# Kernel optimization log

Measured on AMD Instinct MI355X. Metric: run time of the kernel, lower is better.

## Reference

```python
import jax, jax.numpy as jnp
import numpy as np

BN_EPS = 1e-5

def _bn_eval(x, gamma, beta):
    # Fresh torch BatchNorm1d in eval mode: running_mean=0, running_var=1
    return x * (gamma / jnp.sqrt(1.0 + BN_EPS)) + beta

def setup_inputs() -> dict:
    key = jax.random.key(0)
    ks = jax.random.split(key, 10)
    Q, K, H, W, D = 64, 128, 24, 8, 128
    L = H * W            # seq_len = 192
    FF = 2048            # dim_feedforward
    q_feat = jax.random.normal(ks[0], (Q, H, W, D), dtype=jnp.float32)
    g_feat = jax.random.normal(ks[1], (K, H, W, D), dtype=jnp.float32)
    se = jax.random.normal(ks[2], (L, L), dtype=jnp.float32)
    score_embed = (se + se.T).reshape(1, 1, L, L)
    s = 1.0 / np.sqrt(D)
    fc0_w = jax.random.uniform(ks[3], (D, D), jnp.float32, -s, s)
    fc0_b = jax.random.uniform(ks[4], (D,), jnp.float32, -s, s)
    s2 = 1.0 / np.sqrt(L)
    fc2_w = jax.random.uniform(ks[5], (FF, L), jnp.float32, -s2, s2)
    fc2_b = jax.random.uniform(ks[6], (FF,), jnp.float32, -s2, s2)
    s3 = 1.0 / np.sqrt(FF)
    fc3_w = jax.random.uniform(ks[7], (1, FF), jnp.float32, -s3, s3)
    fc3_b = jax.random.uniform(ks[8], (1,), jnp.float32, -s3, s3)
    bn1_g = jnp.ones((1,)); bn1_b = jnp.zeros((1,))
    bn2_g = jnp.ones((FF,)) + 0.1 * jax.random.normal(ks[9], (FF,), jnp.float32)
    bn2_b = jnp.zeros((FF,))
    bn3_g = jnp.ones((1,)); bn3_b = jnp.zeros((1,))
    return dict(q_feat=q_feat, g_feat=g_feat, score_embed=score_embed,
                fc0_w=fc0_w, fc0_b=fc0_b, fc2_w=fc2_w, fc2_b=fc2_b,
                fc3_w=fc3_w, fc3_b=fc3_b, bn1_g=bn1_g, bn1_b=bn1_b,
                bn2_g=bn2_g, bn2_b=bn2_b, bn3_g=bn3_g, bn3_b=bn3_b)

def reference(q_feat, g_feat, score_embed, fc0_w, fc0_b, fc2_w, fc2_b,
              fc3_w, fc3_b, bn1_g, bn1_b, bn2_g, bn2_b, bn3_g, bn3_b):
    Q = q_feat.shape[0]
    K = g_feat.shape[0]
    D = q_feat.shape[-1]
    L = score_embed.shape[-1]  # seq_len
    tgt = q_feat.reshape(Q, L, D)
    mem = g_feat.reshape(K, L, D)
    query = tgt @ fc0_w.T + fc0_b      # [Q, L, D]
    key_ = mem @ fc0_w.T + fc0_b       # [K, L, D]
    # [Q, K, L(s), L(t)] score, modulated by broadcast sigmoid bias
    score = jnp.einsum('qtd,ksd->qkst', query, key_) * jax.nn.sigmoid(score_embed)
    score = score.reshape(Q * K, L, L)
    # max over s and over t, concatenated per pair -> [QK, 2L]
    score = jnp.concatenate([score.max(axis=1), score.max(axis=2)], axis=-1)
    score = score.reshape(-1, L)       # [2*QK, L]
    score = _bn_eval(score, bn1_g, bn1_b)
    score = score @ fc2_w.T + fc2_b    # [2*QK, FF]
    score = _bn_eval(score, bn2_g, bn2_b)
    score = jax.nn.relu(score)
    score = score @ fc3_w.T + fc3_b    # [2*QK, 1]
    score = score.reshape(-1, 2).sum(axis=-1, keepdims=True)  # [QK, 1]
    score = _bn_eval(score, bn3_g, bn3_b)
    return score.reshape(Q, K)
```

## Files before the change

### kernel.cpp

```cpp
#include <hip/hip_runtime.h>

#define LL 192
#define FF 2048

typedef __attribute__((__ext_vector_type__(8)))  __bf16 bf16x8;
typedef __attribute__((__ext_vector_type__(4)))  __bf16 bf16x4;
typedef __attribute__((__ext_vector_type__(4)))  float  f32x4;

#define MFMA16(a, b, c) __builtin_amdgcn_mfma_f32_16x16x32_bf16((a), (b), (c), 0, 0, 0)


__device__ __forceinline__ float fmax_quad(float x) {
    int xi = __builtin_bit_cast(int, x);
    float y = fmaxf(x, __builtin_bit_cast(float,
                  __builtin_amdgcn_mov_dpp(xi, 0xB1, 0xF, 0xF, true)));
    int yi = __builtin_bit_cast(int, y);
    return fmaxf(y, __builtin_bit_cast(float,
                  __builtin_amdgcn_mov_dpp(yi, 0x4E, 0xF, 0xF, true)));
}

__launch_bounds__(256, 2)
__global__ void proj_prep_kernel(const float* __restrict__ qf_in,
                                 const float* __restrict__ gf_in,
                                 const float* __restrict__ fc0w,
                                 const float* __restrict__ fc0b,
                                 const float* __restrict__ se,
                                 const float* __restrict__ fc2w,
                                 const float* __restrict__ fc2b,
                                 const float* __restrict__ bn2g,
                                 const float* __restrict__ bn2b,
                                 const float* __restrict__ fc3w,
                                 __bf16* __restrict__ kfragA,
                                 __bf16* __restrict__ qfrag16,
                                 float* __restrict__ sig32,
                                 __bf16* __restrict__ fc2w_bf,
                                 float* __restrict__ h2,
                                 float* __restrict__ bb2,
                                 float* __restrict__ f3)
{
    int bx = blockIdx.x, tid = threadIdx.x;
    if (bx >= 1152) {
        int i0 = (bx - 1152) * 256 + tid;
        const int stride = 160 * 256;
        const float c1 = rsqrtf(1.f + 1e-5f);
        for (int i = i0; i < LL * LL; i += stride) {
            int r = i & 3, lane = (i >> 2) & 63, tile = i >> 8;
            int jt = tile % 12, st = tile / 12;
            int s = st * 16 + (lane >> 4) * 4 + r;
            int t = jt * 16 + (lane & 15);
            sig32[i] = 1.f / (1.f + __expf(-se[s * 192 + t]));
        }
        for (int i = i0; i < FF * LL; i += stride)
            fc2w_bf[i] = (__bf16)fc2w[i];
        for (int i = i0; i < FF; i += stride) {
            float h = bn2g[i] * c1;
            h2[i]  = h;
            bb2[i] = fc2b[i] * h + bn2b[i];
            f3[i]  = fc3w[i];
        }
        return;
    }
    __shared__ __bf16 Xs[32][136];
    __shared__ __bf16 Ws[128][136];
    __shared__ __bf16 Os[4096];
    const float* src = (bx < 384) ? (qf_in + (size_t)bx * (32 * 128))
                                  : (gf_in + (size_t)(bx - 384) * (32 * 128));
#pragma unroll
    for (int it = 0; it < 4; ++it) {
        int e = (it * 256 + tid) * 4;
        int r = e >> 7, c = e & 127;
        float4 v = *reinterpret_cast<const float4*>(src + e);
        bf16x4 xv;
        xv[0] = (__bf16)v.x; xv[1] = (__bf16)v.y;
        xv[2] = (__bf16)v.z; xv[3] = (__bf16)v.w;
        *reinterpret_cast<bf16x4*>(&Xs[r][c]) = xv;
    }
#pragma unroll
    for (int it = 0; it < 16; ++it) {
        int e = (it * 256 + tid) * 4;
        int r = e >> 7, c = e & 127;
        float4 v = *reinterpret_cast<const float4*>(fc0w + e);
        bf16x4 xv;
        xv[0] = (__bf16)v.x; xv[1] = (__bf16)v.y;
        xv[2] = (__bf16)v.z; xv[3] = (__bf16)v.w;
        *reinterpret_cast<bf16x4*>(&Ws[r][c]) = xv;
    }
    __syncthreads();

    int wv = tid >> 6, lane = tid & 63, quad = lane >> 4, l16 = lane & 15;
    int n0 = wv * 32;
    f32x4 acc[2][2];
#pragma unroll
    for (int m = 0; m < 2; ++m)
#pragma unroll
        for (int n = 0; n < 2; ++n) acc[m][n] = (f32x4){0.f, 0.f, 0.f, 0.f};
#pragma unroll
    for (int ks = 0; ks < 4; ++ks) {
        bf16x8 a0 = *reinterpret_cast<const bf16x8*>(&Xs[l16][ks * 32 + quad * 8]);
        bf16x8 a1 = *reinterpret_cast<const bf16x8*>(&Xs[16 + l16][ks * 32 + quad * 8]);
        bf16x8 b0 = *reinterpret_cast<const bf16x8*>(&Ws[n0 + l16][ks * 32 + quad * 8]);
        bf16x8 b1 = *reinterpret_cast<const bf16x8*>(&Ws[n0 + 16 + l16][ks * 32 + quad * 8]);
        acc[0][0] = MFMA16(a0, b0, acc[0][0]);
        acc[0][1] = MFMA16(a0, b1, acc[0][1]);
        acc[1][0] = MFMA16(a1, b0, acc[1][0]);
        acc[1][1] = MFMA16(a1, b1, acc[1][1]);
    }
#pragma unroll
    for (int mt = 0; mt < 2; ++mt)
#pragma unroll
        for (int nt = 0; nt < 2; ++nt) {
            int d = n0 + nt * 16 + l16;
            float bv = fc0b[d];
            int abase = mt * 2048 + (d >> 5) * 512 + ((d >> 3) & 3) * 128 + (d & 7);
#pragma unroll
            for (int r = 0; r < 4; ++r)
                Os[abase + (quad * 4 + r) * 8] = (__bf16)(acc[mt][nt][r] + bv);
        }
    __syncthreads();

    int row0 = bx * 32;
    __bf16* dst;
    if (bx < 384) {
        int qi = row0 / 192, tg0 = (row0 % 192) >> 4;
        dst = qfrag16 + qi * 24576 + tg0 * 2048;
    } else {
        int rk0 = row0 - 12288;
        int ki = rk0 / 192, sg0 = (rk0 % 192) >> 4;
        dst = kfragA + ki * 24576 + sg0 * 2048;
    }
#pragma unroll
    for (int it = 0; it < 2; ++it) {
        int e = (it * 256 + tid) * 8;
        *reinterpret_cast<bf16x8*>(dst + e) =
            *reinterpret_cast<const bf16x8*>(&Os[e]);
    }
}

__launch_bounds__(256, 1)
__global__ void score_kernel(const __bf16* __restrict__ kfragA,
                             const __bf16* __restrict__ qfrag16,
                             const float* __restrict__ sig32,
                             const float* __restrict__ bn1g,
                             const float* __restrict__ bn1b,
                             __bf16* __restrict__ Sred)
{
    __shared__ __bf16 Abuf[8192];
    __shared__ __bf16 rowT4[2][16][200];

    int tid = threadIdx.x;
    int q0 = (blockIdx.x & 31) * 2;
    int kbase = (blockIdx.x >> 5) << 2;
    int w = tid >> 6, lane = tid & 63, quad = lane >> 4, l16 = lane & 15;
    const float g1c = bn1g[0] * rsqrtf(1.f + 1e-5f);
    const float b1v = bn1b[0];

    bf16x8 Bf[2][3][4];
#pragma unroll
    for (int p = 0; p < 2; ++p) {
        const __bf16* qb = qfrag16 + (size_t)(q0 + p) * 24576 + lane * 8;
#pragma unroll
        for (int j = 0; j < 3; ++j)
#pragma unroll
            for (int ks = 0; ks < 4; ++ks)
                Bf[p][j][ks] = *reinterpret_cast<const bf16x8*>(
                    qb + ((3 * w + j) * 4 + ks) * 512);
    }

#pragma unroll 1
    for (int kk = 0; kk < 4; ++kk) {
        int kidx = kbase + kk;
        const __bf16* kp = kfragA + (size_t)kidx * 24576;
        float cm[2][3];
#pragma unroll
        for (int p = 0; p < 2; ++p)
#pragma unroll
            for (int j = 0; j < 3; ++j) cm[p][j] = -3.0e38f;

#pragma unroll 1
        for (int h = 0; h < 3; ++h) {
#pragma unroll
            for (int it = 0; it < 4; ++it) {
                int e = (it * 256 + tid) * 8;
                *reinterpret_cast<bf16x8*>(&Abuf[e]) =
                    *reinterpret_cast<const bf16x8*>(kp + 8192 * h + e);
            }
            __syncthreads();

#pragma unroll 1
            for (int lsc = 0; lsc < 2; ++lsc) {
                f32x4 acc[2][2][3];
#pragma unroll
                for (int p = 0; p < 2; ++p)
#pragma unroll
                    for (int i = 0; i < 2; ++i)
#pragma unroll
                        for (int j = 0; j < 3; ++j)
                            acc[p][i][j] = (f32x4){0.f, 0.f, 0.f, 0.f};

#pragma unroll
                for (int ks = 0; ks < 4; ++ks) {
                    bf16x8 a0 = *reinterpret_cast<const bf16x8*>(
                        &Abuf[((lsc * 2 + 0) * 4 + ks) * 512 + lane * 8]);
                    bf16x8 a1 = *reinterpret_cast<const bf16x8*>(
                        &Abuf[((lsc * 2 + 1) * 4 + ks) * 512 + lane * 8]);
#pragma unroll
                    for (int j = 0; j < 3; ++j) {
                        acc[0][0][j] = MFMA16(a0, Bf[0][j][ks], acc[0][0][j]);
                        acc[0][1][j] = MFMA16(a1, Bf[0][j][ks], acc[0][1][j]);
                        acc[1][0][j] = MFMA16(a0, Bf[1][j][ks], acc[1][0][j]);
                        acc[1][1][j] = MFMA16(a1, Bf[1][j][ks], acc[1][1][j]);
                    }
                }

#pragma unroll
                for (int i = 0; i < 2; ++i) {
                    int stile = 4 * h + lsc * 2 + i;
                    const float* sp = sig32 +
                        ((size_t)(stile * 12 + 3 * w) * 64 + lane) * 4;
                    f32x4 s0 = *reinterpret_cast<const f32x4*>(sp);
                    f32x4 s1 = *reinterpret_cast<const f32x4*>(sp + 256);
                    f32x4 s2 = *reinterpret_cast<const f32x4*>(sp + 512);
#pragma unroll
                    for (int p = 0; p < 2; ++p) {
                        float v00 = acc[p][i][0][0] * s0[0];
                        float v01 = acc[p][i][0][1] * s0[1];
                        float v02 = acc[p][i][0][2] * s0[2];
                        float v03 = acc[p][i][0][3] * s0[3];
                        float v10 = acc[p][i][1][0] * s1[0];
                        float v11 = acc[p][i][1][1] * s1[1];
                        float v12 = acc[p][i][1][2] * s1[2];
                        float v13 = acc[p][i][1][3] * s1[3];
                        float v20 = acc[p][i][2][0] * s2[0];
                        float v21 = acc[p][i][2][1] * s2[1];
                        float v22 = acc[p][i][2][2] * s2[2];
                        float v23 = acc[p][i][2][3] * s2[3];
                        float rm0 = fmaxf(fmaxf(v00, v10), v20);
                        float rm1 = fmaxf(fmaxf(v01, v11), v21);
                        float rm2 = fmaxf(fmaxf(v02, v12), v22);
                        float rm3 = fmaxf(fmaxf(v03, v13), v23);
                        cm[p][0] = fmaxf(fmaxf(cm[p][0], fmaxf(v00, v01)),
                                         fmaxf(v02, v03));
                        cm[p][1] = fmaxf(fmaxf(cm[p][1], fmaxf(v10, v11)),
                                         fmaxf(v12, v13));
                        cm[p][2] = fmaxf(fmaxf(cm[p][2], fmaxf(v20, v21)),
                                         fmaxf(v22, v23));
                        rm0 = fmax_quad(rm0);
                        rm1 = fmax_quad(rm1);
                        rm2 = fmax_quad(rm2);
                        rm3 = fmax_quad(rm3);
                        if ((l16 & 3) == 0) {
                            bf16x4 pk;
                            pk[0] = (__bf16)rm0; pk[1] = (__bf16)rm1;
                            pk[2] = (__bf16)rm2; pk[3] = (__bf16)rm3;
                            *reinterpret_cast<bf16x4*>(
                                &rowT4[p][(l16 >> 2) * 4 + w]
                                      [stile * 16 + quad * 4]) = pk;
                        }
                    }
                }
            }
            __syncthreads();
        }

#pragma unroll
        for (int p = 0; p < 2; ++p) {
            size_t ob = (size_t)((q0 + p) * 128 + kidx) * 384;
            float v0 = cm[p][0], v1 = cm[p][1], v2 = cm[p][2];
            v0 = fmaxf(v0, __shfl_xor(v0, 16, 64));
            v0 = fmaxf(v0, __shfl_xor(v0, 32, 64));
            v1 = fmaxf(v1, __shfl_xor(v1, 16, 64));
            v1 = fmaxf(v1, __shfl_xor(v1, 32, 64));
            v2 = fmaxf(v2, __shfl_xor(v2, 16, 64));
            v2 = fmaxf(v2, __shfl_xor(v2, 32, 64));
            if (quad == 0) {
                Sred[ob + (3 * w + 0) * 16 + l16] = (__bf16)(v0 * g1c + b1v);
                Sred[ob + (3 * w + 1) * 16 + l16] = (__bf16)(v1 * g1c + b1v);
                Sred[ob + (3 * w + 2) * 16 + l16] = (__bf16)(v2 * g1c + b1v);
            }
        }

        if (tid < 192) {
#pragma unroll
            for (int p = 0; p < 2; ++p) {
                size_t ob = (size_t)((q0 + p) * 128 + kidx) * 384;
                float m1 = -3.0e38f;
#pragma unroll
                for (int c = 0; c < 16; ++c)
                    m1 = fmaxf(m1, (float)rowT4[p][c][tid]);
                Sred[ob + 192 + tid] = (__bf16)(m1 * g1c + b1v);
            }
        }
    }
}

__launch_bounds__(512, 1)
__global__ void mlp_kernel(const __bf16* __restrict__ Sred,
                           const __bf16* __restrict__ fc2w_bf,
                           const float* __restrict__ h2,
                           const float* __restrict__ bb2,
                           const float* __restrict__ f3,
                           const float* __restrict__ fc3b,
                           const float* __restrict__ bn3g,
                           const float* __restrict__ bn3b,
                           float* __restrict__ out)
{
    __shared__ __bf16 As[64][200];
    __shared__ float  psum_lds[8][64];
    int bx = blockIdx.x, tid = threadIdx.x;
    const __bf16* asrc = Sred + (size_t)bx * (64 * 192);
#pragma unroll
    for (int it = 0; it < 3; ++it) {
        int e = (it * 512 + tid) * 8;
        int r = e / 192, c = e - r * 192;
        *reinterpret_cast<bf16x8*>(&As[r][c]) =
            *reinterpret_cast<const bf16x8*>(asrc + e);
    }
    __syncthreads();

    int wv = tid >> 6, lane = tid & 63, quad = lane >> 4, l16 = lane & 15;
    bf16x8 af[4][6];
#pragma unroll
    for (int m = 0; m < 4; ++m)
#pragma unroll
        for (int kk = 0; kk < 6; ++kk)
            af[m][kk] = *reinterpret_cast<const bf16x8*>(
                &As[m * 16 + l16][kk * 32 + quad * 8]);

    float ps[4][4] = {{0.f,0.f,0.f,0.f},{0.f,0.f,0.f,0.f},
                      {0.f,0.f,0.f,0.f},{0.f,0.f,0.f,0.f}};
    for (int nt = 0; nt < 16; ++nt) {
        int n0 = wv * 256 + nt * 16;
        f32x4 acc[4];
#pragma unroll
        for (int m = 0; m < 4; ++m) acc[m] = (f32x4){0.f, 0.f, 0.f, 0.f};
        const __bf16* bp = fc2w_bf + (size_t)(n0 + l16) * 192 + quad * 8;
#pragma unroll
        for (int kk = 0; kk < 6; ++kk) {
            bf16x8 b = *reinterpret_cast<const bf16x8*>(bp + kk * 32);
#pragma unroll
            for (int m = 0; m < 4; ++m) acc[m] = MFMA16(af[m][kk], b, acc[m]);
        }
        int n = n0 + l16;
        float hh = h2[n], bb = bb2[n], ffv = f3[n];
#pragma unroll
        for (int m = 0; m < 4; ++m)
#pragma unroll
            for (int r = 0; r < 4; ++r)
                ps[m][r] += fmaxf(acc[m][r] * hh + bb, 0.f) * ffv;
    }
#pragma unroll
    for (int m = 0; m < 4; ++m)
#pragma unroll
        for (int r = 0; r < 4; ++r) {
            float v = ps[m][r];
            v += __shfl_xor(v, 1, 64);
            v += __shfl_xor(v, 2, 64);
            v += __shfl_xor(v, 4, 64);
            v += __shfl_xor(v, 8, 64);
            if (l16 == 0) psum_lds[wv][m * 16 + quad * 4 + r] = v;
        }
    __syncthreads();
    if (tid < 32) {
        float s = 0.f;
#pragma unroll
        for (int w = 0; w < 8; ++w)
            s += psum_lds[w][2 * tid] + psum_lds[w][2 * tid + 1];
        const float c1 = rsqrtf(1.f + 1e-5f);
        out[bx * 32 + tid] = (s + 2.f * fc3b[0]) * (bn3g[0] * c1) + bn3b[0];
    }
}

extern "C" void kernel_launch(void* const* d_in, const int* in_sizes, int n_in,
                              void* d_out, int out_size, void* d_ws, size_t ws_size,
                              hipStream_t stream)
{
    const float* q_feat = (const float*)d_in[0];
    const float* g_feat = (const float*)d_in[1];
    const float* se     = (const float*)d_in[2];
    const float* fc0w   = (const float*)d_in[3];
    const float* fc0b   = (const float*)d_in[4];
    const float* fc2w   = (const float*)d_in[5];
    const float* fc2b   = (const float*)d_in[6];
    const float* fc3w   = (const float*)d_in[7];
    const float* fc3b   = (const float*)d_in[8];
    const float* bn1g   = (const float*)d_in[9];
    const float* bn1b   = (const float*)d_in[10];
    const float* bn2g   = (const float*)d_in[11];
    const float* bn2b   = (const float*)d_in[12];
    const float* bn3g   = (const float*)d_in[13];
    const float* bn3b   = (const float*)d_in[14];
    float* out = (float*)d_out;

    char* ws = (char*)d_ws;
    __bf16* kfragA   = (__bf16*)(ws);
    __bf16* qfrag16  = (__bf16*)(ws +  6291456);
    float*  sig32    = (float*) (ws +  9437184);
    __bf16* fc2w_bf  = (__bf16*)(ws +  9584640);
    float*  h2       = (float*) (ws + 10371072);
    float*  bb2      = (float*) (ws + 10379264);
    float*  f3       = (float*) (ws + 10387456);
    __bf16* Sred     = (__bf16*)(ws + 10395648);

    proj_prep_kernel<<<1312, 256, 0, stream>>>(q_feat, g_feat, fc0w, fc0b, se,
                                               fc2w, fc2b, bn2g, bn2b, fc3w,
                                               kfragA, qfrag16, sig32, fc2w_bf,
                                               h2, bb2, f3);
    score_kernel<<<1024, 256, 0, stream>>>(kfragA, qfrag16, sig32, bn1g, bn1b, Sred);
    mlp_kernel<<<256, 512, 0, stream>>>(Sred, fc2w_bf, h2, bb2, f3,
                                        fc3b, bn3g, bn3b, out);
}
```

Baseline: 222.1 us.

## Pack row-max reduction into fp16 pairs and load K tiles via async LDS

The row-max epilogue now packs pairs of partial maxima into fp16x2 and reduces them with packed max plus DPP swizzles, halving the cross-lane and LDS reduction work. The final column reduction handles two values per thread. K-fragment tiles are copied straight from global memory into LDS with global_load_lds instead of going through registers, and the lsc loop is fully unrolled. Rounding toward zero to fp16 can overflow or lose precision for large scores before the bf16 output, and the async LDS addressing relies on per-wave base semantics.

```diff
diff --git a/kernel.cpp b/kernel.cpp
--- a/kernel.cpp
+++ b/kernel.cpp
@@ -1,4 +1,5 @@
 #include <hip/hip_runtime.h>
+#include <hip/hip_fp16.h>
 
 #define LL 192
 #define FF 2048
@@ -6,17 +7,27 @@
 typedef __attribute__((__ext_vector_type__(8)))  __bf16 bf16x8;
 typedef __attribute__((__ext_vector_type__(4)))  __bf16 bf16x4;
 typedef __attribute__((__ext_vector_type__(4)))  float  f32x4;
+typedef __attribute__((__ext_vector_type__(2)))  _Float16 f16x2;
 
 #define MFMA16(a, b, c) __builtin_amdgcn_mfma_f32_16x16x32_bf16((a), (b), (c), 0, 0, 0)
 
 
-__device__ __forceinline__ float fmax_quad(float x) {
-    int xi = __builtin_bit_cast(int, x);
-    float y = fmaxf(x, __builtin_bit_cast(float,
-                  __builtin_amdgcn_mov_dpp(xi, 0xB1, 0xF, 0xF, true)));
-    int yi = __builtin_bit_cast(int, y);
-    return fmaxf(y, __builtin_bit_cast(float,
-                  __builtin_amdgcn_mov_dpp(yi, 0x4E, 0xF, 0xF, true)));
+#define ASYNC_LDS16(g, l)                                        \
+    __builtin_amdgcn_global_load_lds(                            \
+        (const __attribute__((address_space(1))) void*)(g),      \
+        (__attribute__((address_space(3))) void*)(l), 16, 0, 0)
+
+template<int CTL>
+__device__ __forceinline__ unsigned dppu(unsigned x) {
+    return (unsigned)__builtin_amdgcn_mov_dpp((int)x, CTL, 0xF, 0xF, true);
+}
+__device__ __forceinline__ unsigned pkrtz_u(float a, float b) {
+    return __builtin_bit_cast(unsigned, __builtin_amdgcn_cvt_pkrtz(a, b));
+}
+__device__ __forceinline__ unsigned hmax2u(unsigned a, unsigned b) {
+    unsigned r;
+    asm("v_pk_max_f16 %0, %1, %2" : "=v"(r) : "v"(a), "v"(b));
+    return r;
 }
 
 __launch_bounds__(256, 2)
@@ -145,7 +156,7 @@
                              __bf16* __restrict__ Sred)
 {
     __shared__ __bf16 Abuf[8192];
-    __shared__ __bf16 rowT4[2][16][200];
+    __shared__ unsigned rowP[2][16][98];
 
     int tid = threadIdx.x;
     int q0 = (blockIdx.x & 31) * 2;
@@ -179,14 +190,12 @@
 #pragma unroll 1
         for (int h = 0; h < 3; ++h) {
 #pragma unroll
-            for (int it = 0; it < 4; ++it) {
-                int e = (it * 256 + tid) * 8;
-                *reinterpret_cast<bf16x8*>(&Abuf[e]) =
-                    *reinterpret_cast<const bf16x8*>(kp + 8192 * h + e);
-            }
+            for (int it = 0; it < 4; ++it)
+                ASYNC_LDS16(kp + 8192 * h + (it * 256 + tid) * 8,
+                            &Abuf[(it * 256 + (tid & 192)) * 8]);
             __syncthreads();
 
-#pragma unroll 1
+#pragma unroll
             for (int lsc = 0; lsc < 2; ++lsc) {
                 f32x4 acc[2][2][3];
 #pragma unroll
@@ -222,39 +231,29 @@
                     f32x4 s2 = *reinterpret_cast<const f32x4*>(sp + 512);
 #pragma unroll
                     for (int p = 0; p < 2; ++p) {
-                        float v00 = acc[p][i][0][0] * s0[0];
-                        float v01 = acc[p][i][0][1] * s0[1];
-                        float v02 = acc[p][i][0][2] * s0[2];
-                        float v03 = acc[p][i][0][3] * s0[3];
-                        float v10 = acc[p][i][1][0] * s1[0];
-                        float v11 = acc[p][i][1][1] * s1[1];
-                        float v12 = acc[p][i][1][2] * s1[2];
-                        float v13 = acc[p][i][1][3] * s1[3];
-                        float v20 = acc[p][i][2][0] * s2[0];
-                        float v21 = acc[p][i][2][1] * s2[1];
-                        float v22 = acc[p][i][2][2] * s2[2];
-                        float v23 = acc[p][i][2][3] * s2[3];
-                        float rm0 = fmaxf(fmaxf(v00, v10), v20);
-                        float rm1 = fmaxf(fmaxf(v01, v11), v21);
-                        float rm2 = fmaxf(fmaxf(v02, v12), v22);
-                        float rm3 = fmaxf(fmaxf(v03, v13), v23);
-                        cm[p][0] = fmaxf(fmaxf(cm[p][0], fmaxf(v00, v01)),
-                                         fmaxf(v02, v03));
-                        cm[p][1] = fmaxf(fmaxf(cm[p][1], fmaxf(v10, v11)),
-                                         fmaxf(v12, v13));
-                        cm[p][2] = fmaxf(fmaxf(cm[p][2], fmaxf(v20, v21)),
-                                         fmaxf(v22, v23));
-                        rm0 = fmax_quad(rm0);
-                        rm1 = fmax_quad(rm1);
-                        rm2 = fmax_quad(rm2);
-                        rm3 = fmax_quad(rm3);
+                        f32x4 v0 = acc[p][i][0] * s0;
+                        f32x4 v1 = acc[p][i][1] * s1;
+                        f32x4 v2 = acc[p][i][2] * s2;
+                        cm[p][0] = fmaxf(fmaxf(cm[p][0], fmaxf(v0[0], v0[1])),
+                                         fmaxf(v0[2], v0[3]));
+                        cm[p][1] = fmaxf(fmaxf(cm[p][1], fmaxf(v1[0], v1[1])),
+                                         fmaxf(v1[2], v1[3]));
+                        cm[p][2] = fmaxf(fmaxf(cm[p][2], fmaxf(v2[0], v2[1])),
+                                         fmaxf(v2[2], v2[3]));
+                        unsigned h01 = pkrtz_u(
+                            fmaxf(fmaxf(v0[0], v1[0]), v2[0]),
+                            fmaxf(fmaxf(v0[1], v1[1]), v2[1]));
+                        unsigned h23 = pkrtz_u(
+                            fmaxf(fmaxf(v0[2], v1[2]), v2[2]),
+                            fmaxf(fmaxf(v0[3], v1[3]), v2[3]));
+                        h01 = hmax2u(h01, dppu<0xB1>(h01));
+                        h01 = hmax2u(h01, dppu<0x4E>(h01));
+                        h23 = hmax2u(h23, dppu<0xB1>(h23));
+                        h23 = hmax2u(h23, dppu<0x4E>(h23));
                         if ((l16 & 3) == 0) {
-                            bf16x4 pk;
-                            pk[0] = (__bf16)rm0; pk[1] = (__bf16)rm1;
-                            pk[2] = (__bf16)rm2; pk[3] = (__bf16)rm3;
-                            *reinterpret_cast<bf16x4*>(
-                                &rowT4[p][(l16 >> 2) * 4 + w]
-                                      [stile * 16 + quad * 4]) = pk;
+                            int rp = stile * 8 + quad * 2;
+                            rowP[p][(l16 >> 2) * 4 + w][rp]     = h01;
+                            rowP[p][(l16 >> 2) * 4 + w][rp + 1] = h23;
                         }
                     }
                 }
@@ -279,15 +278,22 @@
             }
         }
 
-        if (tid < 192) {
+        if (tid < 96) {
 #pragma unroll
             for (int p = 0; p < 2; ++p) {
                 size_t ob = (size_t)((q0 + p) * 128 + kidx) * 384;
-                float m1 = -3.0e38f;
-#pragma unroll
-                for (int c = 0; c < 16; ++c)
-                    m1 = fmaxf(m1, (float)rowT4[p][c][tid]);
-                Sred[ob + 192 + tid] = (__bf16)(m1 * g1c + b1v);
+                unsigned m = rowP[p][0][tid];
+#pragma unroll
+                for (int c = 1; c < 16; ++c)
+                    m = hmax2u(m, rowP[p][c][tid]);
+                __half2 hm = __builtin_bit_cast(__half2, m);
+                float lo = __low2float(hm), hi = __high2float(hm);
+                unsigned two =
+                    (unsigned)__builtin_bit_cast(unsigned short,
+                        (__bf16)(lo * g1c + b1v)) |
+                    ((unsigned)__builtin_bit_cast(unsigned short,
+                        (__bf16)(hi * g1c + b1v)) << 16);
+                *reinterpret_cast<unsigned*>(&Sred[ob + 192 + 2 * tid]) = two;
             }
         }
     }
```

Result: slower. 267.0 us (+20.2%).
